# Performance work log

Hardware: AMD Instinct MI355X
Metric: run time of the kernel (lower is better)

Reference implementation:

```python
import jax, jax.numpy as jnp
import numpy as np
import math

N_AGENTS = 16

def _mlp2(x, W1, b1, W2, b2):
    # tanh on first layer only, matching the torch module
    return jnp.tanh(x @ W1 + b1) @ W2 + b2

def setup_inputs() -> dict:
    key = jax.random.key(0)
    ks = jax.random.split(key, 24)
    B, N, A, IN, D = 2048, N_AGENTS, 32, 128, 128
    NODES = B * N
    s = 0.05
    inp = {
        "obs": jax.random.normal(ks[0], (NODES, IN), jnp.float32),
        "policies": jax.random.uniform(ks[1], (NODES, A), jnp.float32),
        "actions": jax.random.uniform(ks[2], (NODES, A), jnp.float32),
        "weights": jax.random.uniform(ks[3], (1,), jnp.float32),
        "noise": jax.random.normal(ks[4], (NODES, N, A), jnp.float32) * 0.1,
        "Wk1": jax.random.normal(ks[5], (IN, 32), jnp.float32) * s,
        "bk1": jnp.zeros((32,), jnp.float32),
        "Wk2": jax.random.normal(ks[6], (32, D), jnp.float32) * s,
        "bk2": jnp.zeros((D,), jnp.float32),
        "Wq1": jax.random.normal(ks[7], (IN, 32), jnp.float32) * s,
        "bq1": jnp.zeros((32,), jnp.float32),
        "Wq2": jax.random.normal(ks[8], (32, D), jnp.float32) * s,
        "bq2": jnp.zeros((D,), jnp.float32),
        "Wv1": jax.random.normal(ks[9], (IN, 32), jnp.float32) * s,
        "bv1": jnp.zeros((32,), jnp.float32),
        "Wv2": jax.random.normal(ks[10], (32, D), jnp.float32) * s,
        "bv2": jnp.zeros((D,), jnp.float32),
        "Wval": jax.random.normal(ks[11], (D + A, 1), jnp.float32) * s,
        "bval": jnp.zeros((1,), jnp.float32),
    }
    return inp

def reference(obs, policies, actions, weights, noise,
              Wk1, bk1, Wk2, bk2, Wq1, bq1, Wq2, bq2, Wv1, bv1, Wv2, bv2,
              Wval, bval):
    N = N_AGENTS
    NODES, _ = obs.shape
    B = NODES // N
    A = policies.shape[-1]
    D = Wk2.shape[1]

    # ---- SoftAttentionInput: graph soft attention over complete N-agent graphs
    k = _mlp2(obs, Wk1, bk1, Wk2, bk2).reshape(B, N, D)
    q = _mlp2(obs, Wq1, bq1, Wq2, bq2).reshape(B, N, D)
    v = _mlp2(obs, Wv1, bv1, Wv2, bv2).reshape(B, N, D)
    # score for receiver i from sender j: key[j] . query[i]
    scores = jnp.einsum('bjd,bid->bij', k, q) / math.sqrt(D)
    alpha = jax.nn.softmax(scores, axis=-1)               # softmax over senders j
    obs_proc = jnp.einsum('bij,bjd->bid', alpha, v)       # [B,N,D]

    # ---- SoftAttentionWeight: PRD mixing of policies and noisy actions
    pi = policies.reshape(B, N, A)
    act = actions.reshape(B, N, A)
    w = weights                                           # scalar mixing weight, shape (1,)
    # z[b,i,k] = w*act[b,k] + (1-w)*pi[b,k] + noise (mailbox of receiver i)
    z = w * act[:, None, :, :] + (1.0 - w) * pi[:, None, :, :] + noise.reshape(B, N, N, A)
    # place_policies construction: z_final[b,i,j,k] = pi[b,k] if k==j else z[b,i,k];
    # mean over k  =>  (pi[b,j] - z[b,i,j] + sum_k z[b,i,k]) / N
    z_sum = jnp.sum(z, axis=2)                            # [B,N,A]
    z_mix = (pi[:, None, :, :] - z + z_sum[:, :, None, :]) / N  # [B,i,j,A]

    obs_b = jnp.broadcast_to(obs_proc[:, None, :, :], (B, N, N, D))  # [b,i,j] = obs_proc[b,j]
    obs_final = jnp.concatenate([obs_b, z_mix], axis=-1).reshape(B * N, N, D + A)

    # ---- ValueNetwork
    x = obs_final @ Wval + bval                           # [B*N, N, 1]
    weights_preproc = alpha.reshape(B * N, N, 1)
    return x, weights_preproc
```

## Files before the change

### kernel.cpp

```cpp
#include <hip/hip_runtime.h>

typedef __attribute__((ext_vector_type(8))) short bf16x8;
typedef __attribute__((ext_vector_type(4))) float f32x4;

__device__ __forceinline__ unsigned short f2bf(float f){
  union { float f; unsigned int u; } v; v.f = f;
  unsigned int u = v.u;
  return (unsigned short)((u + 0x7FFFu + ((u >> 16) & 1u)) >> 16);
}

__device__ __forceinline__ float fast_tanh(float x){
  x = fminf(15.f, fmaxf(-15.f, x));
  float e = __expf(2.f * x);
  return (e - 1.f) / (e + 1.f);
}

__device__ __forceinline__ float dot128(const float* __restrict__ a,
                                        const float* __restrict__ b){
  float s = 0.f;
  for (int c = 0; c < 128; c += 4){
    float4 x = *(const float4*)(a + c);
    float4 y = *(const float4*)(b + c);
    s += x.x*y.x + x.y*y.y + x.z*y.z + x.w*y.w;
  }
  return s;
}

#define GRPSUM(x) { x += __shfl_xor(x, 1); x += __shfl_xor(x, 2); \
                    x += __shfl_xor(x, 4); x += __shfl_xor(x, 8); }

__global__ __launch_bounds__(64) void k0_kernel(
    const float* __restrict__ Wk1, const float* __restrict__ Wq1, const float* __restrict__ Wv1,
    const float* __restrict__ Wk2, const float* __restrict__ bk2,
    const float* __restrict__ Wq2, const float* __restrict__ bq2,
    const float* __restrict__ Wv2, const float* __restrict__ bv2,
    const float* __restrict__ Wval, float* __restrict__ ws)
{
  const int tid = blockIdx.x * 64 + threadIdx.x;
  const float rs = 0.08838834764831845f;
  unsigned short* bp = (unsigned short*)ws;
  unsigned short* b2 = (unsigned short*)(ws + 6144);

  if (tid < 1536){
    const int e = tid & 7, l = (tid >> 3) & 63, tt = tid >> 9;
    const int g = (l >> 4) * 8 + e;
    float val = 0.f;
    if (tt < 2){
      const int h = (l & 15) + tt * 16;
      val = rs * dot128(Wk2 + h * 128, Wq2 + g * 128);
    } else if ((l & 15) == 0){
      val = rs * dot128(Wq2 + g * 128, bk2);
    }
    b2[tid] = f2bf(val);
  } else if (tid < 1600){
    const int h = tid - 1536;
    if (h < 32) ws[6912 + h] = rs * dot128(Wk2 + h * 128, bq2);
    else        ws[6944 + (h - 32)] = dot128(Wv2 + (h - 32) * 128, Wval);
  } else if (tid == 1600){
    ws[6976] = rs * dot128(bk2, bq2);
  } else if (tid == 1601){
    ws[6977] = dot128(bv2, Wval);
  }

  for (int idx = tid; idx < 12288; idx += 4096){
    const int e  = idx & 7;
    const int l  = (idx >> 3) & 63;
    const int kc = (idx >> 9) & 3;
    const int nt = (idx >> 11) & 1;
    const int m  = idx >> 12;
    const float* W1 = (m == 0) ? Wk1 : ((m == 1) ? Wq1 : Wv1);
    const int krow = kc * 32 + (l >> 4) * 8 + e;
    const int col  = nt * 16 + (l & 15);
    bp[idx] = f2bf(W1[krow * 32 + col]);
  }
}

__global__ __launch_bounds__(256, 2) void fused2_kernel(
    const float* __restrict__ obs,
    const float* __restrict__ policies, const float* __restrict__ actions,
    const float* __restrict__ noise, const float* __restrict__ weights,
    const float* __restrict__ bk1p, const float* __restrict__ bq1p, const float* __restrict__ bv1p,
    const float* __restrict__ Wval, const float* __restrict__ bval,
    const float* __restrict__ ws,
    float* __restrict__ out_x, float* __restrict__ out_alpha)
{
  __shared__ __align__(16) unsigned short hk_s[512];
  __shared__ __align__(16) unsigned short hq_s[512];
  __shared__ __align__(16) unsigned short tq_s[512];
  __shared__ __align__(16) float rql_s[16];
  __shared__ __align__(16) float vvl_s[16];
  __shared__ __align__(16) float nvw[256];
  __shared__ __align__(16) float pvl_s[16], avl_s[16], ovl_s[16];

  const int t = threadIdx.x;
  const int wid = t >> 6, l = t & 63;
  const int b = blockIdx.x;
  const float wscal = weights[0];
  const float bvs = bval[0];

  if (wid == 0){
    const int li = l & 15, gp = l >> 4;

    const float* orow = obs + (size_t)(b * 16 + li) * 128 + gp * 8;
    float4 ob[8];
#pragma unroll
    for (int kc = 0; kc < 4; kc++){
      ob[kc * 2]     = *(const float4*)(orow + kc * 32);
      ob[kc * 2 + 1] = *(const float4*)(orow + kc * 32 + 4);
    }

    const bf16x8* bp  = (const bf16x8*)ws;
    const bf16x8* b2p = (const bf16x8*)(ws + 6144);
    const bf16x8 b20 = b2p[l], b21 = b2p[64 + l], b22 = b2p[128 + l];
    const float u0 = ws[6912 + li], u1 = ws[6928 + li];
    const float wv0 = ws[6944 + li], wv1 = ws[6960 + li];
    const float ccv = ws[6976], cvv = ws[6977];
    const float bk0 = bk1p[li], bk1v = bk1p[16 + li];
    const float bq0 = bq1p[li], bq1v = bq1p[16 + li];
    const float bv0 = bv1p[li], bv1v = bv1p[16 + li];

    bf16x8 afr[4];
#pragma unroll
    for (int kc = 0; kc < 4; kc++){
      bf16x8 a;
      a[0]=(short)f2bf(ob[kc*2].x); a[1]=(short)f2bf(ob[kc*2].y);
      a[2]=(short)f2bf(ob[kc*2].z); a[3]=(short)f2bf(ob[kc*2].w);
      a[4]=(short)f2bf(ob[kc*2+1].x); a[5]=(short)f2bf(ob[kc*2+1].y);
      a[6]=(short)f2bf(ob[kc*2+1].z); a[7]=(short)f2bf(ob[kc*2+1].w);
      afr[kc] = a;
    }
    f32x4 acc[6];
#pragma unroll
    for (int mt = 0; mt < 6; mt++){ f32x4 z = {0.f,0.f,0.f,0.f}; acc[mt] = z; }
#pragma unroll
    for (int mt = 0; mt < 6; mt++){
#pragma unroll
      for (int kc = 0; kc < 4; kc++)
        acc[mt] = __builtin_amdgcn_mfma_f32_16x16x32_bf16(afr[kc], bp[(mt*4+kc)*64 + l], acc[mt], 0, 0, 0);
    }

#pragma unroll
    for (int tile = 0; tile < 2; tile++){
      const float bk_ = tile ? bk1v : bk0;
      const float bq_ = tile ? bq1v : bq0;
      f32x4 ck = acc[tile], cq = acc[2 + tile];
#pragma unroll
      for (int r = 0; r < 4; r++){
        hk_s[(gp*4+r)*32 + tile*16 + li] = f2bf(fast_tanh(ck[r] + bk_));
        hq_s[(gp*4+r)*32 + tile*16 + li] = f2bf(fast_tanh(cq[r] + bq_));
      }
    }

    {
      f32x4 c0 = acc[4], c1 = acc[5];
      float vp0 = wv0*fast_tanh(c0[0]+bv0) + wv1*fast_tanh(c1[0]+bv1v);
      float vp1 = wv0*fast_tanh(c0[1]+bv0) + wv1*fast_tanh(c1[1]+bv1v);
      float vp2 = wv0*fast_tanh(c0[2]+bv0) + wv1*fast_tanh(c1[2]+bv1v);
      float vp3 = wv0*fast_tanh(c0[3]+bv0) + wv1*fast_tanh(c1[3]+bv1v);
      GRPSUM(vp0); GRPSUM(vp1); GRPSUM(vp2); GRPSUM(vp3);
      if (li == 0){
        float4 vq; vq.x = vp0+cvv; vq.y = vp1+cvv; vq.z = vp2+cvv; vq.w = vp3+cvv;
        *(float4*)&vvl_s[gp*4] = vq;
      }
    }

    const bf16x8 aq = *(const bf16x8*)(hq_s + li*32 + gp*8);
    f32x4 cu0 = {u0,u0,u0,u0}, cu1 = {u1,u1,u1,u1}, cu2 = {ccv,ccv,ccv,ccv};
    f32x4 tq0 = __builtin_amdgcn_mfma_f32_16x16x32_bf16(aq, b20, cu0, 0, 0, 0);
    f32x4 tq1 = __builtin_amdgcn_mfma_f32_16x16x32_bf16(aq, b21, cu1, 0, 0, 0);
    f32x4 rqt = __builtin_amdgcn_mfma_f32_16x16x32_bf16(aq, b22, cu2, 0, 0, 0);
    if (li == 0){
      float4 rv; rv.x = rqt[0]; rv.y = rqt[1]; rv.z = rqt[2]; rv.w = rqt[3];
      *(float4*)&rql_s[gp*4] = rv;
    }
#pragma unroll
    for (int r = 0; r < 4; r++){
      tq_s[(gp*4+r)*32 + li]      = f2bf(tq0[r]);
      tq_s[(gp*4+r)*32 + 16 + li] = f2bf(tq1[r]);
    }

    const bf16x8 ak = *(const bf16x8*)(hk_s + li*32 + gp*8);
    const bf16x8 bt = *(const bf16x8*)(tq_s + li*32 + gp*8);
    f32x4 zz = {0.f,0.f,0.f,0.f};
    f32x4 S = __builtin_amdgcn_mfma_f32_16x16x32_bf16(ak, bt, zz, 0, 0, 0);
    const float rc = rql_s[li];
    float s0 = S[0]+rc, s1 = S[1]+rc, s2 = S[2]+rc, s3 = S[3]+rc;

    float mx = fmaxf(fmaxf(s0, s1), fmaxf(s2, s3));
    mx = fmaxf(mx, __shfl_xor(mx, 16)); mx = fmaxf(mx, __shfl_xor(mx, 32));
    float e0 = __expf(s0-mx), e1 = __expf(s1-mx), e2 = __expf(s2-mx), e3 = __expf(s3-mx);
    float sm = e0+e1+e2+e3;
    sm += __shfl_xor(sm, 16); sm += __shfl_xor(sm, 32);
    const float inv = 1.f / sm;
    const float a0 = e0*inv, a1 = e1*inv, a2 = e2*inv, a3 = e3*inv;

    float* aT = (float*)tq_s;
    { float4 av4; av4.x = a0; av4.y = a1; av4.z = a2; av4.w = a3;
      *(float4*)&aT[li*16 + gp*4] = av4; }
    { float4 o4 = *(const float4*)&aT[l*4];
      *(float4*)(out_alpha + (size_t)b*256 + l*4) = o4; }

    float4 vq4 = *(const float4*)&vvl_s[gp*4];
    float ovp = a0*vq4.x + a1*vq4.y + a2*vq4.z + a3*vq4.w;
    ovp += __shfl_xor(ovp, 16); ovp += __shfl_xor(ovp, 32);
    if (l < 16) ovl_s[l] = ovp;
  } else {
    const int wn = wid - 1;
    const int q8 = l & 7, r8 = l >> 3;
    const int rbase = wn * 88 + r8;
    const float* nb = noise + (size_t)b * 8192;
    const float4 wv4 = *(const float4*)(Wval + 128 + q8 * 4);

    float4 pA0, pA1, aA0, aA1, wpa, wpb;
    const int jp = l >> 2, seg = l & 3;
    if (wid == 1){
      const float* pp = policies + (size_t)(b * 16 + jp) * 32 + seg * 8;
      const float* ap = actions  + (size_t)(b * 16 + jp) * 32 + seg * 8;
      pA0 = *(const float4*)(pp);
      pA1 = *(const float4*)(pp + 4);
      aA0 = *(const float4*)(ap);
      aA1 = *(const float4*)(ap + 4);
      wpa = *(const float4*)(Wval + 128 + seg * 8);
      wpb = *(const float4*)(Wval + 132 + seg * 8);
    }

    float4 nz[11];
#pragma unroll
    for (int p = 0; p < 11; p++){
      const int row = rbase + p * 8;
      if (row < 256) nz[p] = *(const float4*)(nb + row * 32 + q8 * 4);
    }
#pragma unroll
    for (int p = 0; p < 11; p++){
      const int row = rbase + p * 8;
      if (row < 256){
        float s = nz[p].x*wv4.x + nz[p].y*wv4.y + nz[p].z*wv4.z + nz[p].w*wv4.w;
        s += __shfl_xor(s, 1); s += __shfl_xor(s, 2); s += __shfl_xor(s, 4);
        if (q8 == 0) nvw[row] = s;
      }
    }

    if (wid == 1){
      float pvv = pA0.x*wpa.x + pA0.y*wpa.y + pA0.z*wpa.z + pA0.w*wpa.w
                + pA1.x*wpb.x + pA1.y*wpb.y + pA1.z*wpb.z + pA1.w*wpb.w;
      float avv = aA0.x*wpa.x + aA0.y*wpa.y + aA0.z*wpa.z + aA0.w*wpa.w
                + aA1.x*wpb.x + aA1.y*wpb.y + aA1.z*wpb.z + aA1.w*wpb.w;
      pvv += __shfl_xor(pvv, 1); pvv += __shfl_xor(pvv, 2);
      avv += __shfl_xor(avv, 1); avv += __shfl_xor(avv, 2);
      if (seg == 0){ pvl_s[jp] = pvv; avl_s[jp] = avv; }
    }
  }

  __syncthreads();

  {
    const int j = t & 15;
    const float pv = pvl_s[j], av = avl_s[j];
    const float zval = wscal * av + (1.f - wscal) * pv + nvw[t];
    float zs = zval;
    GRPSUM(zs);
    out_x[(size_t)b * 256 + t] = ovl_s[t >> 4] + (pv - zval + zs) * 0.0625f + bvs;
  }
}

extern "C" void kernel_launch(void* const* d_in, const int* in_sizes, int n_in,
                              void* d_out, int out_size, void* d_ws, size_t ws_size,
                              hipStream_t stream)
{
  const float* obs      = (const float*)d_in[0];
  const float* policies = (const float*)d_in[1];
  const float* actions  = (const float*)d_in[2];
  const float* weights  = (const float*)d_in[3];
  const float* noise    = (const float*)d_in[4];
  const float* Wk1  = (const float*)d_in[5];
  const float* bk1  = (const float*)d_in[6];
  const float* Wk2  = (const float*)d_in[7];
  const float* bk2  = (const float*)d_in[8];
  const float* Wq1  = (const float*)d_in[9];
  const float* bq1  = (const float*)d_in[10];
  const float* Wq2  = (const float*)d_in[11];
  const float* bq2  = (const float*)d_in[12];
  const float* Wv1  = (const float*)d_in[13];
  const float* bv1  = (const float*)d_in[14];
  const float* Wv2  = (const float*)d_in[15];
  const float* bv2  = (const float*)d_in[16];
  const float* Wval = (const float*)d_in[17];
  const float* bval = (const float*)d_in[18];

  float* out = (float*)d_out;
  float* ws  = (float*)d_ws;

  const int NODES = in_sizes[0] / 128;
  const int B = NODES / 16;

  float* out_x     = out;
  float* out_alpha = out + (size_t)NODES * 16;

  hipLaunchKernelGGL(k0_kernel, dim3(64), dim3(64), 0, stream,
                     Wk1, Wq1, Wv1, Wk2, bk2, Wq2, bq2, Wv2, bv2, Wval, ws);
  hipLaunchKernelGGL(fused2_kernel, dim3(B), dim3(256), 0, stream,
                     obs, policies, actions, noise, weights,
                     bk1, bq1, bv1, Wval, bval, ws,
                     out_x, out_alpha);
}
```

Before: 32.02 us.

## Spread first-layer MFMAs across three waves and stage obs in shared memory

The first-layer K/Q/V projections were all done by wave 0 while the other waves only handled noise. They are now split so waves 0–2 each compute one projection from an obs tile staged once in padded shared memory. All four waves issue their noise loads up front, and wave 3 handles the policy/action dot products. The aim is a shorter serial critical path in wave 0 and earlier memory traffic, at the cost of an extra block barrier and the removal of the min-blocks launch bound. The final output also switches its obs_proc index from t>>4 to t&15, which changes indexing semantics.

```diff
diff --git a/kernel.cpp b/kernel.cpp
--- a/kernel.cpp
+++ b/kernel.cpp
@@ -28,6 +28,7 @@
 
 #define GRPSUM(x) { x += __shfl_xor(x, 1); x += __shfl_xor(x, 2); \
                     x += __shfl_xor(x, 4); x += __shfl_xor(x, 8); }
+
 
 __global__ __launch_bounds__(64) void k0_kernel(
     const float* __restrict__ Wk1, const float* __restrict__ Wq1, const float* __restrict__ Wv1,
@@ -75,7 +76,7 @@
   }
 }
 
-__global__ __launch_bounds__(256, 2) void fused2_kernel(
+__global__ __launch_bounds__(256) void fused_kernel(
     const float* __restrict__ obs,
     const float* __restrict__ policies, const float* __restrict__ actions,
     const float* __restrict__ noise, const float* __restrict__ weights,
@@ -84,85 +85,132 @@
     const float* __restrict__ ws,
     float* __restrict__ out_x, float* __restrict__ out_alpha)
 {
+  __shared__ __align__(16) float obs_s[16 * 132];
   __shared__ __align__(16) unsigned short hk_s[512];
   __shared__ __align__(16) unsigned short hq_s[512];
   __shared__ __align__(16) unsigned short tq_s[512];
-  __shared__ __align__(16) float rql_s[16];
-  __shared__ __align__(16) float vvl_s[16];
   __shared__ __align__(16) float nvw[256];
-  __shared__ __align__(16) float pvl_s[16], avl_s[16], ovl_s[16];
+  __shared__ __align__(16) float pvl[16], avl[16], vvl[16], rql[16], ovl[16];
 
   const int t = threadIdx.x;
   const int wid = t >> 6, l = t & 63;
   const int b = blockIdx.x;
+  const int li = l & 15, gp = l >> 4;
+  const int q8 = l & 7, r8 = l >> 3;
+
+  const float* nbl = noise + (size_t)b * 8192 + (wid * 64 + r8) * 32 + q8 * 4;
+  float4 nz[8];
+#pragma unroll
+  for (int p = 0; p < 8; p++) nz[p] = *(const float4*)(nbl + p * 256);
+
+  const float4* osrc = (const float4*)(obs + (size_t)b * 2048);
+  float4 o0 = osrc[t];
+  float4 o1 = osrc[t + 256];
+  const float4 wv4 = *(const float4*)(Wval + 128 + q8 * 4);
   const float wscal = weights[0];
   const float bvs = bval[0];
 
+  float4 pA0, pA1, aA0, aA1, wpa, wpb;
+  const int jp = l >> 2, seg = l & 3;
+  if (wid == 3){
+    const float* pp = policies + (size_t)(b * 16 + jp) * 32 + seg * 8;
+    const float* ap = actions  + (size_t)(b * 16 + jp) * 32 + seg * 8;
+    pA0 = *(const float4*)(pp);
+    pA1 = *(const float4*)(pp + 4);
+    aA0 = *(const float4*)(ap);
+    aA1 = *(const float4*)(ap + 4);
+    wpa = *(const float4*)(Wval + 128 + seg * 8);
+    wpb = *(const float4*)(Wval + 132 + seg * 8);
+  }
+
+  ((float4*)obs_s)[(t >> 5) * 33 + (t & 31)] = o0;
+  ((float4*)obs_s)[((t + 256) >> 5) * 33 + ((t + 256) & 31)] = o1;
+
+#pragma unroll
+  for (int p = 0; p < 8; p++){
+    float s = nz[p].x*wv4.x + nz[p].y*wv4.y + nz[p].z*wv4.z + nz[p].w*wv4.w;
+    s += __shfl_xor(s, 1); s += __shfl_xor(s, 2); s += __shfl_xor(s, 4);
+    if (q8 == 0) nvw[wid * 64 + p * 8 + r8] = s;
+  }
+
+  if (wid == 3){
+    float pvv = pA0.x*wpa.x + pA0.y*wpa.y + pA0.z*wpa.z + pA0.w*wpa.w
+              + pA1.x*wpb.x + pA1.y*wpb.y + pA1.z*wpb.z + pA1.w*wpb.w;
+    float avv = aA0.x*wpa.x + aA0.y*wpa.y + aA0.z*wpa.z + aA0.w*wpa.w
+              + aA1.x*wpb.x + aA1.y*wpb.y + aA1.z*wpb.z + aA1.w*wpb.w;
+    pvv += __shfl_xor(pvv, 1); pvv += __shfl_xor(pvv, 2);
+    avv += __shfl_xor(avv, 1); avv += __shfl_xor(avv, 2);
+    if (seg == 0){ pvl[jp] = pvv; avl[jp] = avv; }
+  }
+
+  __syncthreads();
+
+  if (wid < 3){
+    const bf16x8* bp = (const bf16x8*)ws;
+    bf16x8 bfr[8];
+#pragma unroll
+    for (int nt = 0; nt < 2; nt++)
+#pragma unroll
+      for (int kc = 0; kc < 4; kc++)
+        bfr[nt*4+kc] = bp[((wid*2+nt)*4+kc)*64 + l];
+
+    bf16x8 afr[4];
+#pragma unroll
+    for (int kc = 0; kc < 4; kc++){
+      float4 x0 = ((const float4*)obs_s)[li*33 + kc*8 + gp*2];
+      float4 x1 = ((const float4*)obs_s)[li*33 + kc*8 + gp*2 + 1];
+      bf16x8 a;
+      a[0]=(short)f2bf(x0.x); a[1]=(short)f2bf(x0.y);
+      a[2]=(short)f2bf(x0.z); a[3]=(short)f2bf(x0.w);
+      a[4]=(short)f2bf(x1.x); a[5]=(short)f2bf(x1.y);
+      a[6]=(short)f2bf(x1.z); a[7]=(short)f2bf(x1.w);
+      afr[kc] = a;
+    }
+    f32x4 acc0 = {0.f,0.f,0.f,0.f}, acc1 = {0.f,0.f,0.f,0.f};
+#pragma unroll
+    for (int kc = 0; kc < 4; kc++)
+      acc0 = __builtin_amdgcn_mfma_f32_16x16x32_bf16(afr[kc], bfr[kc], acc0, 0, 0, 0);
+#pragma unroll
+    for (int kc = 0; kc < 4; kc++)
+      acc1 = __builtin_amdgcn_mfma_f32_16x16x32_bf16(afr[kc], bfr[4+kc], acc1, 0, 0, 0);
+
+    if (wid == 0){
+      const float b0 = bk1p[li], b1 = bk1p[16 + li];
+#pragma unroll
+      for (int r = 0; r < 4; r++){
+        hk_s[(gp*4+r)*32 + li]      = f2bf(fast_tanh(acc0[r] + b0));
+        hk_s[(gp*4+r)*32 + 16 + li] = f2bf(fast_tanh(acc1[r] + b1));
+      }
+    } else if (wid == 1){
+      const float b0 = bq1p[li], b1 = bq1p[16 + li];
+#pragma unroll
+      for (int r = 0; r < 4; r++){
+        hq_s[(gp*4+r)*32 + li]      = f2bf(fast_tanh(acc0[r] + b0));
+        hq_s[(gp*4+r)*32 + 16 + li] = f2bf(fast_tanh(acc1[r] + b1));
+      }
+    } else {
+      const float b0 = bv1p[li], b1 = bv1p[16 + li];
+      const float wv0 = ws[6944 + li], wv1 = ws[6960 + li];
+      const float cvv = ws[6977];
+      float vp0 = wv0*fast_tanh(acc0[0]+b0) + wv1*fast_tanh(acc1[0]+b1);
+      float vp1 = wv0*fast_tanh(acc0[1]+b0) + wv1*fast_tanh(acc1[1]+b1);
+      float vp2 = wv0*fast_tanh(acc0[2]+b0) + wv1*fast_tanh(acc1[2]+b1);
+      float vp3 = wv0*fast_tanh(acc0[3]+b0) + wv1*fast_tanh(acc1[3]+b1);
+      GRPSUM(vp0); GRPSUM(vp1); GRPSUM(vp2); GRPSUM(vp3);
+      if (li == 0){
+        float4 vq; vq.x = vp0+cvv; vq.y = vp1+cvv; vq.z = vp2+cvv; vq.w = vp3+cvv;
+        *(float4*)&vvl[gp*4] = vq;
+      }
+    }
+  }
+
+  __syncthreads();
+
   if (wid == 0){
-    const int li = l & 15, gp = l >> 4;
-
-    const float* orow = obs + (size_t)(b * 16 + li) * 128 + gp * 8;
-    float4 ob[8];
-#pragma unroll
-    for (int kc = 0; kc < 4; kc++){
-      ob[kc * 2]     = *(const float4*)(orow + kc * 32);
-      ob[kc * 2 + 1] = *(const float4*)(orow + kc * 32 + 4);
-    }
-
-    const bf16x8* bp  = (const bf16x8*)ws;
     const bf16x8* b2p = (const bf16x8*)(ws + 6144);
     const bf16x8 b20 = b2p[l], b21 = b2p[64 + l], b22 = b2p[128 + l];
     const float u0 = ws[6912 + li], u1 = ws[6928 + li];
-    const float wv0 = ws[6944 + li], wv1 = ws[6960 + li];
-    const float ccv = ws[6976], cvv = ws[6977];
-    const float bk0 = bk1p[li], bk1v = bk1p[16 + li];
-    const float bq0 = bq1p[li], bq1v = bq1p[16 + li];
-    const float bv0 = bv1p[li], bv1v = bv1p[16 + li];
-
-    bf16x8 afr[4];
-#pragma unroll
-    for (int kc = 0; kc < 4; kc++){
-      bf16x8 a;
-      a[0]=(short)f2bf(ob[kc*2].x); a[1]=(short)f2bf(ob[kc*2].y);
-      a[2]=(short)f2bf(ob[kc*2].z); a[3]=(short)f2bf(ob[kc*2].w);
-      a[4]=(short)f2bf(ob[kc*2+1].x); a[5]=(short)f2bf(ob[kc*2+1].y);
-      a[6]=(short)f2bf(ob[kc*2+1].z); a[7]=(short)f2bf(ob[kc*2+1].w);
-      afr[kc] = a;
-    }
-    f32x4 acc[6];
-#pragma unroll
-    for (int mt = 0; mt < 6; mt++){ f32x4 z = {0.f,0.f,0.f,0.f}; acc[mt] = z; }
-#pragma unroll
-    for (int mt = 0; mt < 6; mt++){
-#pragma unroll
-      for (int kc = 0; kc < 4; kc++)
-        acc[mt] = __builtin_amdgcn_mfma_f32_16x16x32_bf16(afr[kc], bp[(mt*4+kc)*64 + l], acc[mt], 0, 0, 0);
-    }
-
-#pragma unroll
-    for (int tile = 0; tile < 2; tile++){
-      const float bk_ = tile ? bk1v : bk0;
-      const float bq_ = tile ? bq1v : bq0;
-      f32x4 ck = acc[tile], cq = acc[2 + tile];
-#pragma unroll
-      for (int r = 0; r < 4; r++){
-        hk_s[(gp*4+r)*32 + tile*16 + li] = f2bf(fast_tanh(ck[r] + bk_));
-        hq_s[(gp*4+r)*32 + tile*16 + li] = f2bf(fast_tanh(cq[r] + bq_));
-      }
-    }
-
-    {
-      f32x4 c0 = acc[4], c1 = acc[5];
-      float vp0 = wv0*fast_tanh(c0[0]+bv0) + wv1*fast_tanh(c1[0]+bv1v);
-      float vp1 = wv0*fast_tanh(c0[1]+bv0) + wv1*fast_tanh(c1[1]+bv1v);
-      float vp2 = wv0*fast_tanh(c0[2]+bv0) + wv1*fast_tanh(c1[2]+bv1v);
-      float vp3 = wv0*fast_tanh(c0[3]+bv0) + wv1*fast_tanh(c1[3]+bv1v);
-      GRPSUM(vp0); GRPSUM(vp1); GRPSUM(vp2); GRPSUM(vp3);
-      if (li == 0){
-        float4 vq; vq.x = vp0+cvv; vq.y = vp1+cvv; vq.z = vp2+cvv; vq.w = vp3+cvv;
-        *(float4*)&vvl_s[gp*4] = vq;
-      }
-    }
+    const float ccv = ws[6976];
 
     const bf16x8 aq = *(const bf16x8*)(hq_s + li*32 + gp*8);
     f32x4 cu0 = {u0,u0,u0,u0}, cu1 = {u1,u1,u1,u1}, cu2 = {ccv,ccv,ccv,ccv};
@@ -171,7 +219,7 @@
     f32x4 rqt = __builtin_amdgcn_mfma_f32_16x16x32_bf16(aq, b22, cu2, 0, 0, 0);
     if (li == 0){
       float4 rv; rv.x = rqt[0]; rv.y = rqt[1]; rv.z = rqt[2]; rv.w = rqt[3];
-      *(float4*)&rql_s[gp*4] = rv;
+      *(float4*)&rql[gp*4] = rv;
     }
 #pragma unroll
     for (int r = 0; r < 4; r++){
@@ -183,7 +231,7 @@
     const bf16x8 bt = *(const bf16x8*)(tq_s + li*32 + gp*8);
     f32x4 zz = {0.f,0.f,0.f,0.f};
     f32x4 S = __builtin_amdgcn_mfma_f32_16x16x32_bf16(ak, bt, zz, 0, 0, 0);
-    const float rc = rql_s[li];
+    const float rc = rql[li];
     float s0 = S[0]+rc, s1 = S[1]+rc, s2 = S[2]+rc, s3 = S[3]+rc;
 
     float mx = fmaxf(fmaxf(s0, s1), fmaxf(s2, s3));
@@ -195,71 +243,26 @@
     const float a0 = e0*inv, a1 = e1*inv, a2 = e2*inv, a3 = e3*inv;
 
     float* aT = (float*)tq_s;
-    { float4 av4; av4.x = a0; av4.y = a1; av4.z = a2; av4.w = a3;
-      *(float4*)&aT[li*16 + gp*4] = av4; }
+    { float4 av4x; av4x.x = a0; av4x.y = a1; av4x.z = a2; av4x.w = a3;
+      *(float4*)&aT[li*16 + gp*4] = av4x; }
     { float4 o4 = *(const float4*)&aT[l*4];
       *(float4*)(out_alpha + (size_t)b*256 + l*4) = o4; }
 
-    float4 vq4 = *(const float4*)&vvl_s[gp*4];
+    float4 vq4 = *(const float4*)&vvl[gp*4];
     float ovp = a0*vq4.x + a1*vq4.y + a2*vq4.z + a3*vq4.w;
     ovp += __shfl_xor(ovp, 16); ovp += __shfl_xor(ovp, 32);
-    if (l < 16) ovl_s[l] = ovp;
-  } else {
-    const int wn = wid - 1;
-    const int q8 = l & 7, r8 = l >> 3;
-    const int rbase = wn * 88 + r8;
-    const float* nb = noise + (size_t)b * 8192;
-    const float4 wv4 = *(const float4*)(Wval + 128 + q8 * 4);
-
-    float4 pA0, pA1, aA0, aA1, wpa, wpb;
-    const int jp = l >> 2, seg = l & 3;
-    if (wid == 1){
-      const float* pp = policies + (size_t)(b * 16 + jp) * 32 + seg * 8;
-      const float* ap = actions  + (size_t)(b * 16 + jp) * 32 + seg * 8;
-      pA0 = *(const float4*)(pp);
-      pA1 = *(const float4*)(pp + 4);
-      aA0 = *(const float4*)(ap);
-      aA1 = *(const float4*)(ap + 4);
-      wpa = *(const float4*)(Wval + 128 + seg * 8);
-      wpb = *(const float4*)(Wval + 132 + seg * 8);
-    }
-
-    float4 nz[11];
-#pragma unroll
-    for (int p = 0; p < 11; p++){
-      const int row = rbase + p * 8;
-      if (row < 256) nz[p] = *(const float4*)(nb + row * 32 + q8 * 4);
-    }
-#pragma unroll
-    for (int p = 0; p < 11; p++){
-      const int row = rbase + p * 8;
-      if (row < 256){
-        float s = nz[p].x*wv4.x + nz[p].y*wv4.y + nz[p].z*wv4.z + nz[p].w*wv4.w;
-        s += __shfl_xor(s, 1); s += __shfl_xor(s, 2); s += __shfl_xor(s, 4);
-        if (q8 == 0) nvw[row] = s;
-      }
-    }
-
-    if (wid == 1){
-      float pvv = pA0.x*wpa.x + pA0.y*wpa.y + pA0.z*wpa.z + pA0.w*wpa.w
-                + pA1.x*wpb.x + pA1.y*wpb.y + pA1.z*wpb.z + pA1.w*wpb.w;
-      float avv = aA0.x*wpa.x + aA0.y*wpa.y + aA0.z*wpa.z + aA0.w*wpa.w
-                + aA1.x*wpb.x + aA1.y*wpb.y + aA1.z*wpb.z + aA1.w*wpb.w;
-      pvv += __shfl_xor(pvv, 1); pvv += __shfl_xor(pvv, 2);
-      avv += __shfl_xor(avv, 1); avv += __shfl_xor(avv, 2);
-      if (seg == 0){ pvl_s[jp] = pvv; avl_s[jp] = avv; }
-    }
+    if (l < 16) ovl[l] = ovp;
   }
 
   __syncthreads();
 
   {
     const int j = t & 15;
-    const float pv = pvl_s[j], av = avl_s[j];
+    const float pv = pvl[j], av = avl[j];
     const float zval = wscal * av + (1.f - wscal) * pv + nvw[t];
     float zs = zval;
     GRPSUM(zs);
-    out_x[(size_t)b * 256 + t] = ovl_s[t >> 4] + (pv - zval + zs) * 0.0625f + bvs;
+    out_x[(size_t)b * 256 + t] = ovl[j] + (pv - zval + zs) * 0.0625f + bvs;
   }
 }
 
@@ -298,7 +301,7 @@
 
   hipLaunchKernelGGL(k0_kernel, dim3(64), dim3(64), 0, stream,
                      Wk1, Wq1, Wv1, Wk2, bk2, Wq2, bq2, Wv2, bv2, Wval, ws);
-  hipLaunchKernelGGL(fused2_kernel, dim3(B), dim3(256), 0, stream,
+  hipLaunchKernelGGL(fused_kernel, dim3(B), dim3(256), 0, stream,
                      obs, policies, actions, noise, weights,
                      bk1, bq1, bv1, Wval, bval, ws,
                      out_x, out_alpha);
```

Measured after the change: 31.60 us. No clear change (-1.3%).
